# Kernel optimization log

Hardware: AMD Instinct MI355X
Metric: run time of the kernel (lower is better)

The kernel has to match this reference:

```python
import jax, jax.numpy as jnp
import numpy as np
import math

CW = 10
T_S = 2.0


def _K(t0):
    t = t0 - CW // 2
    if t < 0:
        return -0.5 * math.exp(t / (T_S / 2.0))
    return math.exp(-t / T_S)

K_VALS = np.array([_K(k) for k in range(CW)], dtype=np.float32)          # synaptic kernel
KS_VALS = np.array([math.exp(-k / T_S) for k in range(CW)], dtype=np.float32)  # spike kernel


def swish(v):
    # original Swish: x * sigmoid(10*x)
    return v * jax.nn.sigmoid(10.0 * v)


def act_fun(v):
    # smooth surrogate spike activation: sigmoid(10*(mem - 0.5)), thresh=0.5
    return jax.nn.sigmoid(10.0 * (v - 0.5))


def setup_inputs() -> dict:
    key = jax.random.key(0)
    k1, k2, k3, k4 = jax.random.split(key, 4)
    B, T = 4096, 50
    x = jax.random.uniform(k1, (B, T, 620), dtype=jnp.float32)
    W1 = jax.random.normal(k2, (200, 620), dtype=jnp.float32) / np.sqrt(620.0)
    W2 = jax.random.normal(k3, (100, 200), dtype=jnp.float32) / np.sqrt(200.0)
    W3 = jax.random.normal(k4, (11, 100), dtype=jnp.float32) / np.sqrt(100.0)
    return {"x": x, "W1": W1, "W2": W2, "W3": W3}


def reference(x, W1, W2, W3):
    B, T, _ = x.shape
    kv = jnp.asarray(K_VALS)
    ks_tail = jnp.asarray(KS_VALS[1:])   # k=1..9; k=0 spike term is always 0 (buffer not yet written)
    kv_tail = jnp.asarray(K_VALS[1:])    # k=1..9 for layer-input history

    # h1 is purely feedforward in time -> precompute, then causal conv with K over CW window.
    h1 = swish(jnp.einsum('btd,nd->btn', x, W1))            # [B, T, 200]
    h1_pad = jnp.pad(h1, ((0, 0), (CW - 1, 0), (0, 0)))
    syn2 = sum(kv[k] * h1_pad[:, CW - 1 - k: CW - 1 - k + T] for k in range(CW))  # [B, T, 200]

    def shift(hist, new):
        # hist[:, j] holds value at time t-1-j; prepend current value
        return jnp.concatenate([new[:, None], hist[:, :-1]], axis=1)

    def step(carry, syn2_t):
        sl2_h, h2_h, sl3_h, h3_h, sl4_h, acc = carry
        # layer 2
        mem2 = syn2_t - jnp.einsum('k,bkn->bn', ks_tail, sl2_h)
        s2 = act_fun(mem2)
        sl2 = s2 * mem2
        h2 = swish(s2 @ W2.T)                                # [B, 100]
        # layer 3
        mem3 = kv[0] * h2 + jnp.einsum('k,bkn->bn', kv_tail, h2_h) \
               - jnp.einsum('k,bkn->bn', ks_tail, sl3_h)
        s3 = act_fun(mem3)
        sl3 = s3 * mem3
        h3 = swish(s3 @ W3.T)                                # [B, 11]
        # layer 4 (output)
        mem4 = kv[0] * h3 + jnp.einsum('k,bkn->bn', kv_tail, h3_h) \
               - jnp.einsum('k,bkn->bn', ks_tail, sl4_h)
        s4 = act_fun(mem4)
        sl4 = s4 * mem4
        carry = (shift(sl2_h, sl2), shift(h2_h, h2), shift(sl3_h, sl3),
                 shift(h3_h, h3), shift(sl4_h, sl4), acc + s4)
        return carry, None

    z = lambda n: jnp.zeros((B, CW - 1, n), dtype=x.dtype)
    carry0 = (z(200), z(100), z(100), z(11), z(11), jnp.zeros((B, 11), dtype=x.dtype))
    carry, _ = jax.lax.scan(step, carry0, jnp.swapaxes(syn2, 0, 1))
    h4_sumspike = carry[-1]
    return h4_sumspike / 50.0
```

## Files before the change

### kernel.cpp

```cpp
#include <hip/hip_runtime.h>
#include <math.h>

#define T_STEPS 50
#define D_IN    620
#define N1      200
#define N2      100
#define N3      11
#define BATCH   4096

typedef short bf16x8 __attribute__((ext_vector_type(8)));
typedef float f32x4  __attribute__((ext_vector_type(4)));

__device__ __constant__ float KV[10] = {
    -0.0033689735f, -0.0091578194f, -0.0248935342f, -0.0676676416f, -0.1839397206f,
     1.0f,           0.6065306597f,  0.3678794412f,  0.2231301601f,  0.1353352832f };

#define RHO    0.60653066f
#define RHO5   0.0820849986f
#define RHO10  0.0067379470f
#define KV0    (-0.0033689735f)
#define C1     (-0.0091578194f)
#define C2     (-0.0248935342f)
#define C3     (-0.0676676416f)
#define C4     (-0.1839397206f)

__device__ __forceinline__ float sigm10(float x) { return 1.0f / (1.0f + __expf(-10.0f * x)); }
__device__ __forceinline__ float swishf(float v) { return v / (1.0f + __expf(-10.0f * v)); }

__device__ __forceinline__ void split2(float x, unsigned short& hi, unsigned short& lo) {
    unsigned u = __float_as_uint(x);
    hi = (unsigned short)(u >> 16);
    float rem = x - __uint_as_float(u & 0xFFFF0000u);
    lo = (unsigned short)(__float_as_uint(rem) >> 16);
}

__global__ void prep_w1(const float* __restrict__ W1, unsigned short* __restrict__ W1pre) {
    int i = blockIdx.x * 256 + threadIdx.x;
    if (i >= 286720) return;
    int kk = i & 31;
    int t1 = i >> 5;
    int r  = t1 % 112;
    int t2 = t1 / 112;
    int p  = t2 & 1;
    int nb = (t2 >> 1) & 1;
    int kt = t2 >> 2;
    int n  = nb * 112 + r;
    int k  = kt * 32 + kk;
    float w = (n < N1 && k < D_IN) ? W1[n * D_IN + k] : 0.0f;
    unsigned short hi, lo; split2(w, hi, lo);
    int gsw = (kk >> 3) ^ ((r >> 1) & 3);
    int idx = kt * 14336 + nb * 7168 + p * 3584 + r * 32 + gsw * 8 + (kk & 7);
    W1pre[idx] = p ? lo : hi;
}

__global__ void prep_w2(const float* __restrict__ W2, unsigned short* __restrict__ W2pre2) {
    int i = blockIdx.x * 256 + threadIdx.x;
    if (i >= 57344) return;
    int e  = i & 7;
    int r  = i >> 3;
    int l  = r & 63;
    int r2 = r >> 6;
    int p  = r2 & 1;
    int r3 = r2 >> 1;
    int ks = r3 % 7;
    int wv = r3 / 7;
    int n  = wv * 16 + (l & 15);
    int k  = ks * 32 + (l >> 4) * 8 + e;
    float v = (n < N2 && k < N1) ? W2[n * N1 + k] : 0.0f;
    unsigned short hi, lo; split2(v, hi, lo);
    W2pre2[i] = p ? lo : hi;
}

__global__ __launch_bounds__(256, 4) void gemm1_mfma(const float* __restrict__ x,
                                                     const unsigned short* __restrict__ W1pre,
                                                     float* __restrict__ h1) {
    __shared__ unsigned short Bs[2][7168];

    const int tid = threadIdx.x;
    const int w   = tid >> 6;
    const int l   = tid & 63;
    const int j   = l >> 4;
    const int r16 = l & 15;
    const int mb  = blockIdx.x >> 1;
    const int nb  = blockIdx.x & 1;
    const long row0 = (long)mb * 128;
    const float* arow0 = x + (row0 + w * 32 + r16) * D_IN;
    const float* arow1 = arow0 + 16 * D_IN;

    f32x4 acc[2][7];
#pragma unroll
    for (int mt = 0; mt < 2; ++mt)
#pragma unroll
        for (int nt = 0; nt < 7; ++nt) acc[mt][nt] = (f32x4){0.f, 0.f, 0.f, 0.f};

    auto stageB = [&](int kt, int bb) {
        const unsigned short* src = W1pre + kt * 14336 + nb * 7168;
#pragma unroll
        for (int it = 0; it < 3; ++it) {
            int ch = it * 256 + tid;
            __builtin_amdgcn_global_load_lds(
                (const __attribute__((address_space(1))) unsigned int*)(src + ch * 8),
                (__attribute__((address_space(3))) unsigned int*)(&Bs[bb][0] + ch * 8), 16, 0, 0);
        }
        if (tid < 128) {
            int ch = 768 + tid;
            __builtin_amdgcn_global_load_lds(
                (const __attribute__((address_space(1))) unsigned int*)(src + ch * 8),
                (__attribute__((address_space(3))) unsigned int*)(&Bs[bb][0] + ch * 8), 16, 0, 0);
        }
    };

    auto loadA = [&](int kt, float (&av)[2][8]) {
#pragma unroll
        for (int mt = 0; mt < 2; ++mt) {
            const float* ar = mt ? arow1 : arow0;
            if (kt < 19) {
                const float* p = ar + kt * 32 + j * 8;
                const float4 u0 = *(const float4*)p;
                const float4 u1 = *(const float4*)(p + 4);
                av[mt][0] = u0.x; av[mt][1] = u0.y; av[mt][2] = u0.z; av[mt][3] = u0.w;
                av[mt][4] = u1.x; av[mt][5] = u1.y; av[mt][6] = u1.z; av[mt][7] = u1.w;
            } else if (j == 0) {
                const float4 u0 = *(const float4*)(ar + 608);
                const float4 u1 = *(const float4*)(ar + 612);
                av[mt][0] = u0.x; av[mt][1] = u0.y; av[mt][2] = u0.z; av[mt][3] = u0.w;
                av[mt][4] = u1.x; av[mt][5] = u1.y; av[mt][6] = u1.z; av[mt][7] = u1.w;
            } else if (j == 1) {
                const float4 u0 = *(const float4*)(ar + 616);
                av[mt][0] = u0.x; av[mt][1] = u0.y; av[mt][2] = u0.z; av[mt][3] = u0.w;
                av[mt][4] = 0.f; av[mt][5] = 0.f; av[mt][6] = 0.f; av[mt][7] = 0.f;
            } else {
#pragma unroll
                for (int e = 0; e < 8; ++e) av[mt][e] = 0.f;
            }
        }
    };

    auto computeKt = [&](float (&av)[2][8], int cur) {
        bf16x8 ah[2], al[2];
#pragma unroll
        for (int mt = 0; mt < 2; ++mt)
#pragma unroll
            for (int e = 0; e < 8; ++e) {
                unsigned short hi, lo; split2(av[mt][e], hi, lo);
                ah[mt][e] = (short)hi; al[mt][e] = (short)lo;
            }
        const unsigned short* B = &Bs[cur][0];
#pragma unroll
        for (int nt = 0; nt < 7; ++nt) {
            const int n  = nt * 16 + r16;
            const int gs = j ^ ((n >> 1) & 3);
            const bf16x8 bh = *(const bf16x8*)(B + n * 32 + gs * 8);
            const bf16x8 bl = *(const bf16x8*)(B + 3584 + n * 32 + gs * 8);
            acc[0][nt] = __builtin_amdgcn_mfma_f32_16x16x32_bf16(ah[0], bh, acc[0][nt], 0, 0, 0);
            acc[1][nt] = __builtin_amdgcn_mfma_f32_16x16x32_bf16(ah[1], bh, acc[1][nt], 0, 0, 0);
            acc[0][nt] = __builtin_amdgcn_mfma_f32_16x16x32_bf16(ah[0], bl, acc[0][nt], 0, 0, 0);
            acc[1][nt] = __builtin_amdgcn_mfma_f32_16x16x32_bf16(ah[1], bl, acc[1][nt], 0, 0, 0);
            acc[0][nt] = __builtin_amdgcn_mfma_f32_16x16x32_bf16(al[0], bh, acc[0][nt], 0, 0, 0);
            acc[1][nt] = __builtin_amdgcn_mfma_f32_16x16x32_bf16(al[1], bh, acc[1][nt], 0, 0, 0);
        }
    };

    float avA[2][8], avB[2][8];
    stageB(0, 0);
    loadA(0, avA);
    __syncthreads();

#pragma unroll 1
    for (int kt = 0; kt < 20; kt += 2) {
        stageB(kt + 1, 1);
        loadA(kt + 1, avB);
        computeKt(avA, 0);
        __syncthreads();
        if (kt + 2 < 20) { stageB(kt + 2, 0); loadA(kt + 2, avA); }
        computeKt(avB, 1);
        __syncthreads();
    }

#pragma unroll
    for (int mt = 0; mt < 2; ++mt) {
        const long grow0 = row0 + w * 32 + mt * 16 + j * 4;
#pragma unroll
        for (int nt = 0; nt < 7; ++nt) {
            const int gcol = nb * 112 + nt * 16 + r16;
            if (gcol < N1) {
#pragma unroll
                for (int q = 0; q < 4; ++q)
                    h1[(grow0 + q) * N1 + gcol] = swishf(acc[mt][nt][q]);
            }
        }
    }
}

__global__ __launch_bounds__(256) void conv_k(float* __restrict__ buf) {
    __shared__ float h1s[T_STEPS * N1];
    const int b = blockIdx.x, tid = threadIdx.x;
    float* p = buf + (size_t)b * (T_STEPS * N1);
    for (int i = tid; i < T_STEPS * N1 / 4; i += 256)
        ((float4*)h1s)[i] = ((const float4*)p)[i];
    __syncthreads();
    for (int i = tid; i < T_STEPS * N1; i += 256) {
        int t = i / N1, n = i - t * N1;
        float s = 0.0f;
#pragma unroll
        for (int k = 0; k < 10; ++k)
            if (k <= t) s = fmaf(KV[k], h1s[(t - k) * N1 + n], s);
        p[i] = s;
    }
}

__global__ __launch_bounds__(512, 2) void snn_scan5(const float* __restrict__ syn2,
                                                    const unsigned short* __restrict__ W2pre2,
                                                    const float* __restrict__ W3,
                                                    float* __restrict__ out) {
    __shared__ __align__(16) unsigned short s2A[8192];
    __shared__ __align__(16) float h2buf[8][132];
    __shared__ __align__(16) float s3buf[8][104];
    __shared__ __align__(16) float W3s[N3 * N2];
    __shared__ __align__(16) float pbuf[8][4][12];

    const int tid = threadIdx.x;
    const int wv  = tid >> 6;
    const int l   = tid & 63;
    const int m16 = l & 15;
    const int j2  = l >> 4;
    const int g   = wv;
    const int c   = l;
    const long b  = (long)blockIdx.x * 8 + g;

    for (int i = tid; i < N3 * N2; i += 512) W3s[i] = W3[i];
    for (int i = tid; i < 8192; i += 512) s2A[i] = 0;

    bf16x8 bh[7], bl[7];
    {
        const unsigned short* wp = W2pre2 + wv * 7168 + l * 8;
#pragma unroll
        for (int ks = 0; ks < 7; ++ks) {
            bh[ks] = *(const bf16x8*)(wp + ks * 1024);
            bl[ks] = *(const bf16x8*)(wp + ks * 1024 + 512);
        }
    }

    const int NL2 = (c < 8)  ? 4 : 3;
    const int NL3 = (c < 36) ? 2 : 1;
    const int o4  = c % 11;
    const int p4  = c / 11;
    const int kbeg = (p4 == 0) ? 0 : (4 + 24 * p4);
    const int nf4  = (p4 == 0) ? 7 : 6;

    float sl2h[10][4] = {}; float Ssl2[4] = {};
    float h2h[10][2]  = {}; float Dd3[2]  = {};
    float sl3h[10][2] = {}; float Ssl3[2] = {};
    float h3h[10]     = {}; float Dd4 = 0.f;
    float sl4h[10]    = {}; float Ssl4 = 0.f;
    float accum       = 0.0f;

    const float* syn2b = syn2 + b * (T_STEPS * N1);
    float syn_nxt[4];
#pragma unroll
    for (int jj = 0; jj < 4; ++jj) syn_nxt[jj] = (jj < NL2) ? syn2b[c + 64 * jj] : 0.0f;

    __syncthreads();

#pragma unroll 1
    for (int tb = 0; tb < T_STEPS; tb += 10) {
#pragma unroll
        for (int u = 0; u < 10; ++u) {
            const int t   = tb + u;
            const int um1 = (u + 9) % 10;
            const int um2 = (u + 8) % 10;
            const int um3 = (u + 7) % 10;
            const int um4 = (u + 6) % 10;
            const int um5 = (u + 5) % 10;

            float syn_cur[4];
#pragma unroll
            for (int jj = 0; jj < 4; ++jj) syn_cur[jj] = syn_nxt[jj];
            if (t + 1 < T_STEPS) {
#pragma unroll
                for (int jj = 0; jj < 4; ++jj)
                    if (jj < NL2) syn_nxt[jj] = syn2b[(t + 1) * N1 + c + 64 * jj];
            }

#pragma unroll
            for (int jj = 0; jj < 4; ++jj) {
                if (jj < NL2) {
                    const int n = c + 64 * jj;
                    const float slp = sl2h[um1][jj];
                    const float slo = sl2h[u][jj];
                    Ssl2[jj] = RHO * (Ssl2[jj] + slp) - RHO10 * slo;
                    const float mem2 = syn_cur[jj] - Ssl2[jj];
                    const float s2   = sigm10(mem2 - 0.5f);
                    sl2h[u][jj] = s2 * mem2;
                    unsigned short hi, lo; split2(s2, hi, lo);
                    const int off = g * 256 + (((n >> 3) ^ (g & 7)) * 8) + (n & 7);
                    s2A[off]        = hi;
                    s2A[4096 + off] = lo;
                }
            }
            __syncthreads();

            {
                f32x4 a0 = (f32x4){0.f, 0.f, 0.f, 0.f};
                f32x4 a1 = (f32x4){0.f, 0.f, 0.f, 0.f};
                const int swz = m16 & 7;
#pragma unroll
                for (int ks = 0; ks < 7; ++ks) {
                    const int gr = (4 * ks + j2) ^ swz;
                    const bf16x8 ahv = *(const bf16x8*)&s2A[m16 * 256 + gr * 8];
                    const bf16x8 alv = *(const bf16x8*)&s2A[4096 + m16 * 256 + gr * 8];
                    if (ks & 1) {
                        a1 = __builtin_amdgcn_mfma_f32_16x16x32_bf16(ahv, bh[ks], a1, 0, 0, 0);
                        a1 = __builtin_amdgcn_mfma_f32_16x16x32_bf16(alv, bh[ks], a1, 0, 0, 0);
                        a1 = __builtin_amdgcn_mfma_f32_16x16x32_bf16(ahv, bl[ks], a1, 0, 0, 0);
                    } else {
                        a0 = __builtin_amdgcn_mfma_f32_16x16x32_bf16(ahv, bh[ks], a0, 0, 0, 0);
                        a0 = __builtin_amdgcn_mfma_f32_16x16x32_bf16(alv, bh[ks], a0, 0, 0, 0);
                        a0 = __builtin_amdgcn_mfma_f32_16x16x32_bf16(ahv, bl[ks], a0, 0, 0, 0);
                    }
                }
                const f32x4 a = a0 + a1;
                if (j2 < 2) {
#pragma unroll
                    for (int q = 0; q < 4; ++q)
                        h2buf[j2 * 4 + q][wv * 16 + m16] = swishf(a[q]);
                }
            }
            __syncthreads();

#pragma unroll
            for (int jj = 0; jj < 2; ++jj) {
                if (jj < NL3) {
                    const int m = c + 64 * jj;
                    const float hm = h2buf[g][m];
                    float gneg = C1 * h2h[um1][jj];
                    gneg = fmaf(C2, h2h[um2][jj], gneg);
                    gneg = fmaf(C3, h2h[um3][jj], gneg);
                    gneg = fmaf(C4, h2h[um4][jj], gneg);
                    Dd3[jj] = fmaf(RHO, Dd3[jj], h2h[um5][jj]);
                    Dd3[jj] = fmaf(-RHO5, h2h[u][jj], Dd3[jj]);
                    const float slp = sl3h[um1][jj];
                    const float slo = sl3h[u][jj];
                    Ssl3[jj] = RHO * (Ssl3[jj] + slp) - RHO10 * slo;
                    const float mem3 = fmaf(KV0, hm, gneg) + Dd3[jj] - Ssl3[jj];
                    const float s3   = sigm10(mem3 - 0.5f);
                    sl3h[u][jj] = s3 * mem3;
                    h2h[u][jj]  = hm;
                    s3buf[g][m] = s3;
                }
            }
            asm volatile("s_waitcnt lgkmcnt(0)" ::: "memory");
            __builtin_amdgcn_sched_barrier(0);

            if (c < 44) {
                float part = 0.0f;
#pragma unroll
                for (int i = 0; i < 7; ++i) {
                    if (i < nf4) {
                        const float4 sv  = *(const float4*)&s3buf[g][kbeg + 4 * i];
                        const float4 wv4 = *(const float4*)&W3s[o4 * N2 + kbeg + 4 * i];
                        part = fmaf(sv.x, wv4.x, part);
                        part = fmaf(sv.y, wv4.y, part);
                        part = fmaf(sv.z, wv4.z, part);
                        part = fmaf(sv.w, wv4.w, part);
                    }
                }
                pbuf[g][p4][o4] = part;
            }
            asm volatile("s_waitcnt lgkmcnt(0)" ::: "memory");
            __builtin_amdgcn_sched_barrier(0);

            if (c < N3) {
                const float a4 = pbuf[g][0][c] + pbuf[g][1][c] + pbuf[g][2][c] + pbuf[g][3][c];
                const float h3 = swishf(a4);
                float gneg = C1 * h3h[um1];
                gneg = fmaf(C2, h3h[um2], gneg);
                gneg = fmaf(C3, h3h[um3], gneg);
                gneg = fmaf(C4, h3h[um4], gneg);
                Dd4 = fmaf(RHO, Dd4, h3h[um5]);
                Dd4 = fmaf(-RHO5, h3h[u], Dd4);
                const float slp = sl4h[um1];
                const float slo = sl4h[u];
                Ssl4 = RHO * (Ssl4 + slp) - RHO10 * slo;
                const float mem4 = fmaf(KV0, h3, gneg) + Dd4 - Ssl4;
                const float s4   = sigm10(mem4 - 0.5f);
                sl4h[u] = s4 * mem4;
                h3h[u]  = h3;
                accum += s4;
            }
        }
    }

    if (c < N3) out[b * N3 + c] = accum * 0.02f;
}

extern "C" void kernel_launch(void* const* d_in, const int* in_sizes, int n_in,
                              void* d_out, int out_size, void* d_ws, size_t ws_size,
                              hipStream_t stream) {
    const float* x  = (const float*)d_in[0];
    const float* W1 = (const float*)d_in[1];
    const float* W2 = (const float*)d_in[2];
    const float* W3 = (const float*)d_in[3];
    float* out = (float*)d_out;

    float* buf = (float*)d_ws;
    unsigned short* W1pre  = (unsigned short*)(buf + (size_t)BATCH * T_STEPS * N1);
    unsigned short* W2pre2 = W1pre + 286720;

    prep_w1<<<1120, 256, 0, stream>>>(W1, W1pre);
    prep_w2<<<224, 256, 0, stream>>>(W2, W2pre2);
    gemm1_mfma<<<3200, 256, 0, stream>>>(x, W1pre, buf);
    conv_k<<<BATCH, 256, 0, stream>>>(buf);
    snn_scan5<<<BATCH / 8, 512, 0, stream>>>(buf, W2pre2, W3, out);
}
```

Before: 582.4 us.

## Cover full N in gemm1 block with 8 waves and triple-buffered B pipeline

Reworks the first GEMM so each 512-thread block computes all 208 padded output columns for 128 rows, with each wave owning 16 rows and 13 N-tiles. Previously the N dimension was split across two blocks. The change removes the second read of x and the 200-to-224 column padding waste. W1 staging becomes a 3-deep LDS ring with explicit vmcnt waits and one barrier per k-step instead of two __syncthreads per pair of steps. In exchange the block uses about 80KB of LDS and more accumulator registers, which may reduce occupancy.

```diff
diff --git a/kernel.cpp b/kernel.cpp
--- a/kernel.cpp
+++ b/kernel.cpp
@@ -36,20 +36,18 @@
 
 __global__ void prep_w1(const float* __restrict__ W1, unsigned short* __restrict__ W1pre) {
     int i = blockIdx.x * 256 + threadIdx.x;
-    if (i >= 286720) return;
+    if (i >= 266240) return;
     int kk = i & 31;
     int t1 = i >> 5;
-    int r  = t1 % 112;
-    int t2 = t1 / 112;
+    int n  = t1 % 208;
+    int t2 = t1 / 208;
     int p  = t2 & 1;
-    int nb = (t2 >> 1) & 1;
-    int kt = t2 >> 2;
-    int n  = nb * 112 + r;
+    int kt = t2 >> 1;
     int k  = kt * 32 + kk;
     float w = (n < N1 && k < D_IN) ? W1[n * D_IN + k] : 0.0f;
     unsigned short hi, lo; split2(w, hi, lo);
-    int gsw = (kk >> 3) ^ ((r >> 1) & 3);
-    int idx = kt * 14336 + nb * 7168 + p * 3584 + r * 32 + gsw * 8 + (kk & 7);
+    int gsw = (kk >> 3) ^ ((n >> 1) & 3);
+    int idx = kt * 13312 + p * 6656 + n * 32 + gsw * 8 + (kk & 7);
     W1pre[idx] = p ? lo : hi;
 }
 
@@ -71,123 +69,112 @@
     W2pre2[i] = p ? lo : hi;
 }
 
-__global__ __launch_bounds__(256, 4) void gemm1_mfma(const float* __restrict__ x,
+__global__ __launch_bounds__(512, 4) void gemm1_mfma(const float* __restrict__ x,
                                                      const unsigned short* __restrict__ W1pre,
                                                      float* __restrict__ h1) {
-    __shared__ unsigned short Bs[2][7168];
+    __shared__ unsigned short Bs[3][13312];
 
     const int tid = threadIdx.x;
     const int w   = tid >> 6;
     const int l   = tid & 63;
     const int j   = l >> 4;
     const int r16 = l & 15;
-    const int mb  = blockIdx.x >> 1;
-    const int nb  = blockIdx.x & 1;
-    const long row0 = (long)mb * 128;
-    const float* arow0 = x + (row0 + w * 32 + r16) * D_IN;
-    const float* arow1 = arow0 + 16 * D_IN;
-
-    f32x4 acc[2][7];
-#pragma unroll
-    for (int mt = 0; mt < 2; ++mt)
-#pragma unroll
-        for (int nt = 0; nt < 7; ++nt) acc[mt][nt] = (f32x4){0.f, 0.f, 0.f, 0.f};
+    const long row0 = (long)blockIdx.x * 128;
+    const float* arow = x + (row0 + w * 16 + r16) * D_IN;
+
+    f32x4 acc[13];
+#pragma unroll
+    for (int nt = 0; nt < 13; ++nt) acc[nt] = (f32x4){0.f, 0.f, 0.f, 0.f};
 
     auto stageB = [&](int kt, int bb) {
-        const unsigned short* src = W1pre + kt * 14336 + nb * 7168;
+        const unsigned short* src = W1pre + kt * 13312;
+        unsigned short* dst = &Bs[bb][0];
 #pragma unroll
         for (int it = 0; it < 3; ++it) {
-            int ch = it * 256 + tid;
+            int ch = it * 512 + tid;
             __builtin_amdgcn_global_load_lds(
                 (const __attribute__((address_space(1))) unsigned int*)(src + ch * 8),
-                (__attribute__((address_space(3))) unsigned int*)(&Bs[bb][0] + ch * 8), 16, 0, 0);
+                (__attribute__((address_space(3))) unsigned int*)(dst + ch * 8), 16, 0, 0);
         }
         if (tid < 128) {
-            int ch = 768 + tid;
+            int ch = 1536 + tid;
             __builtin_amdgcn_global_load_lds(
                 (const __attribute__((address_space(1))) unsigned int*)(src + ch * 8),
-                (__attribute__((address_space(3))) unsigned int*)(&Bs[bb][0] + ch * 8), 16, 0, 0);
+                (__attribute__((address_space(3))) unsigned int*)(dst + ch * 8), 16, 0, 0);
         }
     };
 
-    auto loadA = [&](int kt, float (&av)[2][8]) {
-#pragma unroll
-        for (int mt = 0; mt < 2; ++mt) {
-            const float* ar = mt ? arow1 : arow0;
-            if (kt < 19) {
-                const float* p = ar + kt * 32 + j * 8;
-                const float4 u0 = *(const float4*)p;
-                const float4 u1 = *(const float4*)(p + 4);
-                av[mt][0] = u0.x; av[mt][1] = u0.y; av[mt][2] = u0.z; av[mt][3] = u0.w;
-                av[mt][4] = u1.x; av[mt][5] = u1.y; av[mt][6] = u1.z; av[mt][7] = u1.w;
-            } else if (j == 0) {
-                const float4 u0 = *(const float4*)(ar + 608);
-                const float4 u1 = *(const float4*)(ar + 612);
-                av[mt][0] = u0.x; av[mt][1] = u0.y; av[mt][2] = u0.z; av[mt][3] = u0.w;
-                av[mt][4] = u1.x; av[mt][5] = u1.y; av[mt][6] = u1.z; av[mt][7] = u1.w;
-            } else if (j == 1) {
-                const float4 u0 = *(const float4*)(ar + 616);
-                av[mt][0] = u0.x; av[mt][1] = u0.y; av[mt][2] = u0.z; av[mt][3] = u0.w;
-                av[mt][4] = 0.f; av[mt][5] = 0.f; av[mt][6] = 0.f; av[mt][7] = 0.f;
-            } else {
-#pragma unroll
-                for (int e = 0; e < 8; ++e) av[mt][e] = 0.f;
-            }
-        }
+    auto loadA = [&](int kt, float* av) {
+        const float* p = arow + kt * 32 + j * 8;
+        const float4 u0 = *(const float4*)p;
+        const float4 u1 = *(const float4*)(p + 4);
+        av[0] = u0.x; av[1] = u0.y; av[2] = u0.z; av[3] = u0.w;
+        av[4] = u1.x; av[5] = u1.y; av[6] = u1.z; av[7] = u1.w;
     };
-
-    auto computeKt = [&](float (&av)[2][8], int cur) {
-        bf16x8 ah[2], al[2];
-#pragma unroll
-        for (int mt = 0; mt < 2; ++mt)
-#pragma unroll
-            for (int e = 0; e < 8; ++e) {
-                unsigned short hi, lo; split2(av[mt][e], hi, lo);
-                ah[mt][e] = (short)hi; al[mt][e] = (short)lo;
-            }
-        const unsigned short* B = &Bs[cur][0];
-#pragma unroll
-        for (int nt = 0; nt < 7; ++nt) {
+    auto loadAtail = [&](float* av) {
+        if (j == 0) {
+            const float4 u0 = *(const float4*)(arow + 608);
+            const float4 u1 = *(const float4*)(arow + 612);
+            av[0] = u0.x; av[1] = u0.y; av[2] = u0.z; av[3] = u0.w;
+            av[4] = u1.x; av[5] = u1.y; av[6] = u1.z; av[7] = u1.w;
+        } else if (j == 1) {
+            const float4 u0 = *(const float4*)(arow + 616);
+            av[0] = u0.x; av[1] = u0.y; av[2] = u0.z; av[3] = u0.w;
+            av[4] = 0.f; av[5] = 0.f; av[6] = 0.f; av[7] = 0.f;
+        } else {
+#pragma unroll
+            for (int e = 0; e < 8; ++e) av[e] = 0.f;
+        }
+    };
+
+    float av[2][8];
+    stageB(0, 0);
+    stageB(1, 1);
+    loadA(0, av[0]);
+    loadA(1, av[1]);
+    asm volatile("s_waitcnt vmcnt(7)" ::: "memory");
+    asm volatile("s_barrier" ::: "memory");
+
+#pragma unroll 1
+    for (int kt = 0; kt < 20; ++kt) {
+        bf16x8 ah, al;
+#pragma unroll
+        for (int e = 0; e < 8; ++e) {
+            unsigned short hi, lo; split2(av[kt & 1][e], hi, lo);
+            ah[e] = (short)hi; al[e] = (short)lo;
+        }
+        if (kt < 18) {
+            if (kt + 2 == 19) loadAtail(av[kt & 1]); else loadA(kt + 2, av[kt & 1]);
+            stageB(kt + 2, (kt + 2) % 3);
+        }
+        const unsigned short* B = &Bs[kt % 3][0];
+#pragma unroll
+        for (int nt = 0; nt < 13; ++nt) {
             const int n  = nt * 16 + r16;
             const int gs = j ^ ((n >> 1) & 3);
             const bf16x8 bh = *(const bf16x8*)(B + n * 32 + gs * 8);
-            const bf16x8 bl = *(const bf16x8*)(B + 3584 + n * 32 + gs * 8);
-            acc[0][nt] = __builtin_amdgcn_mfma_f32_16x16x32_bf16(ah[0], bh, acc[0][nt], 0, 0, 0);
-            acc[1][nt] = __builtin_amdgcn_mfma_f32_16x16x32_bf16(ah[1], bh, acc[1][nt], 0, 0, 0);
-            acc[0][nt] = __builtin_amdgcn_mfma_f32_16x16x32_bf16(ah[0], bl, acc[0][nt], 0, 0, 0);
-            acc[1][nt] = __builtin_amdgcn_mfma_f32_16x16x32_bf16(ah[1], bl, acc[1][nt], 0, 0, 0);
-            acc[0][nt] = __builtin_amdgcn_mfma_f32_16x16x32_bf16(al[0], bh, acc[0][nt], 0, 0, 0);
-            acc[1][nt] = __builtin_amdgcn_mfma_f32_16x16x32_bf16(al[1], bh, acc[1][nt], 0, 0, 0);
-        }
-    };
-
-    float avA[2][8], avB[2][8];
-    stageB(0, 0);
-    loadA(0, avA);
-    __syncthreads();
-
-#pragma unroll 1
-    for (int kt = 0; kt < 20; kt += 2) {
-        stageB(kt + 1, 1);
-        loadA(kt + 1, avB);
-        computeKt(avA, 0);
-        __syncthreads();
-        if (kt + 2 < 20) { stageB(kt + 2, 0); loadA(kt + 2, avA); }
-        computeKt(avB, 1);
-        __syncthreads();
+            const bf16x8 bl = *(const bf16x8*)(B + 6656 + n * 32 + gs * 8);
+            acc[nt] = __builtin_amdgcn_mfma_f32_16x16x32_bf16(ah, bh, acc[nt], 0, 0, 0);
+            acc[nt] = __builtin_amdgcn_mfma_f32_16x16x32_bf16(ah, bl, acc[nt], 0, 0, 0);
+            acc[nt] = __builtin_amdgcn_mfma_f32_16x16x32_bf16(al, bh, acc[nt], 0, 0, 0);
+        }
+        if (kt < 18) {
+            asm volatile("s_waitcnt vmcnt(5)" ::: "memory");
+            asm volatile("s_barrier" ::: "memory");
+        } else if (kt == 18) {
+            asm volatile("s_waitcnt vmcnt(0)" ::: "memory");
+            asm volatile("s_barrier" ::: "memory");
+        }
     }
 
 #pragma unroll
-    for (int mt = 0; mt < 2; ++mt) {
-        const long grow0 = row0 + w * 32 + mt * 16 + j * 4;
-#pragma unroll
-        for (int nt = 0; nt < 7; ++nt) {
-            const int gcol = nb * 112 + nt * 16 + r16;
-            if (gcol < N1) {
-#pragma unroll
-                for (int q = 0; q < 4; ++q)
-                    h1[(grow0 + q) * N1 + gcol] = swishf(acc[mt][nt][q]);
-            }
+    for (int nt = 0; nt < 13; ++nt) {
+        const int gcol = nt * 16 + r16;
+        if (gcol < N1) {
+            const long grow0 = row0 + w * 16 + j * 4;
+#pragma unroll
+            for (int q = 0; q < 4; ++q)
+                h1[(grow0 + q) * N1 + gcol] = swishf(acc[nt][q]);
         }
     }
 }
@@ -405,11 +392,11 @@
 
     float* buf = (float*)d_ws;
     unsigned short* W1pre  = (unsigned short*)(buf + (size_t)BATCH * T_STEPS * N1);
-    unsigned short* W2pre2 = W1pre + 286720;
-
-    prep_w1<<<1120, 256, 0, stream>>>(W1, W1pre);
+    unsigned short* W2pre2 = W1pre + 266240;
+
+    prep_w1<<<1040, 256, 0, stream>>>(W1, W1pre);
     prep_w2<<<224, 256, 0, stream>>>(W2, W2pre2);
-    gemm1_mfma<<<3200, 256, 0, stream>>>(x, W1pre, buf);
+    gemm1_mfma<<<1600, 512, 0, stream>>>(x, W1pre, buf);
     conv_k<<<BATCH, 256, 0, stream>>>(buf);
     snn_scan5<<<BATCH / 8, 512, 0, stream>>>(buf, W2pre2, W3, out);
 }
```

Measured after the change: 529.7 us. -9.0%, faster.
